# Kernel optimization log

Measured on AMD Instinct MI355X. Metric: run time of the kernel, lower is better.

## Reference

```python
import jax, jax.numpy as jnp
import numpy as np

K = 16        # max_points
S = 3         # num_scales
D_MODEL = 256
KDIM = 16
TAU = 1e-4
B_BATCH = 512


def _boundaries(k):
    edges = [(i, j) for i in range(k) for j in range(i + 1, k)]
    tris = [(i, j, kk) for i in range(k) for j in range(i + 1, k) for kk in range(j + 1, k)]
    E, T = len(edges), len(tris)
    B1 = np.zeros((k, E), np.float32)
    for e, (i, j) in enumerate(edges):
        B1[i, e] = -1.0
        B1[j, e] = 1.0
    e2i = {e: idx for idx, e in enumerate(edges)}
    B2 = np.zeros((E, T), np.float32)
    for t, (i, j, kk) in enumerate(tris):
        B2[e2i[(j, kk)], t] = 1.0
        B2[e2i[(i, kk)], t] = -1.0
        B2[e2i[(i, j)], t] = 1.0
    e_i = np.array([e[0] for e in edges], np.int32)
    e_j = np.array([e[1] for e in edges], np.int32)
    t_ij = np.array([e2i[(a, b)] for (a, b, c) in tris], np.int32)
    t_jk = np.array([e2i[(b, c)] for (a, b, c) in tris], np.int32)
    t_ik = np.array([e2i[(a, c)] for (a, b, c) in tris], np.int32)
    return B1, B2, e_i, e_j, t_ij, t_jk, t_ik


def setup_inputs() -> dict:
    key = jax.random.key(0)
    ks = jax.random.split(key, 8)
    d = D_MODEL
    B1, B2, e_i, e_j, t_ij, t_jk, t_ik = _boundaries(K)

    def lin(kk, fin, fout):
        return jax.random.normal(kk, (fin, fout), jnp.float32) / np.sqrt(fin).astype(np.float32)

    return dict(
        x=jax.random.normal(ks[0], (B_BATCH, K, d), jnp.float32),
        mask=jnp.ones((B_BATCH, K), jnp.float32),
        B1=jnp.asarray(B1), B2=jnp.asarray(B2), abs_B1=jnp.asarray(np.abs(B1)),
        e_i=jnp.asarray(e_i), e_j=jnp.asarray(e_j),
        t_ij=jnp.asarray(t_ij), t_jk=jnp.asarray(t_jk), t_ik=jnp.asarray(t_ik),
        log_scales=jnp.linspace(-1.5, 1.5, S).astype(jnp.float32),
        Wg=lin(ks[1], d, KDIM), bg=jnp.zeros((KDIM,), jnp.float32),
        Wv0=lin(ks[2], d, d * S), bv0=jnp.zeros((d * S,), jnp.float32),
        We=lin(ks[3], d, d * S), be=jnp.zeros((d * S,), jnp.float32),
        Wout=lin(ks[4], 2 * S * d, d), bout=jnp.zeros((d,), jnp.float32),
        g1=jnp.ones((d,), jnp.float32), b1=jnp.zeros((d,), jnp.float32),
        g2=jnp.ones((d,), jnp.float32), b2=jnp.zeros((d,), jnp.float32),
        Wf1=lin(ks[5], d, 4 * d), bf1=jnp.zeros((4 * d,), jnp.float32),
        Wf2=lin(ks[6], 4 * d, d), bf2=jnp.zeros((d,), jnp.float32),
    )


def _layernorm(x, g, b):
    mu = jnp.mean(x, -1, keepdims=True)
    var = jnp.mean(jnp.square(x - mu), -1, keepdims=True)
    return (x - mu) * jax.lax.rsqrt(var + 1e-5) * g + b


def _forward(x, mask, B1, B2, abs_B1, e_i, e_j, t_ij, t_jk, t_ik,
             log_scales, Wg, bg, Wv0, bv0, We, be, Wout, bout,
             g1, b1, g2, b2, Wf1, bf1, Wf2, bf2):
    B, Kp, d = x.shape
    E = B1.shape[1]
    residual = x
    x_norm = _layernorm(x, g1, b1)
    P = x_norm @ Wg + bg                                   # (B,K,k_dim)
    mask2 = mask[:, :, None] * mask[:, None, :]            # (B,K,K)
    # cdist (safe sqrt: zero diag, no NaN grads)
    pn = jnp.sum(P * P, -1)
    d2 = jnp.maximum(pn[:, :, None] + pn[:, None, :] - 2.0 * jnp.einsum('bik,bjk->bij', P, P), 0.0)
    Dm = jnp.where(d2 > 0, jnp.sqrt(jnp.where(d2 > 0, d2, 1.0)), 0.0) * mask2
    sigma_sq = jnp.square(jnp.exp(log_scales))             # (S,)
    A = jnp.exp(-(Dm * Dm)[:, None] / (2.0 * sigma_sq[None, :, None, None] + 1e-8)) * mask2[:, None]  # (B,S,K,K)
    W1 = A[:, :, e_i, e_j]                                 # (B,S,E) edge gather
    W2 = W1[:, :, t_ij] * W1[:, :, t_jk] * W1[:, :, t_ik]  # (B,S,T) triangle weights
    V0 = (x_norm @ Wv0 + bv0).reshape(B, Kp, S, d).transpose(0, 2, 1, 3)         # (B,S,K,d)
    E_raw = jnp.einsum('ke,bkd->bed', abs_B1, x_norm)                            # (B,E,d)
    E_in = (E_raw @ We + be).reshape(B, E, S, d).transpose(0, 2, 1, 3)           # (B,S,E,d)
    # L0 = B1 diag(W1) B1^T + tau I
    L0 = jnp.einsum('ke,bse,me->bskm', B1, W1, B1) + TAU * jnp.eye(Kp, dtype=x.dtype)
    M0 = jnp.einsum('bskm,bsmd->bskd', L0, V0)
    # L1 = B1^T diag(mask) B1 + B2 diag(W2) B2^T + tau I
    term_down = jnp.einsum('ke,bk,kf->bef', B1, mask, B1)                        # (B,E,E)
    term_up = jnp.einsum('et,bst,ft->bsef', B2, W2, B2)                          # (B,S,E,E)
    L1 = term_down[:, None] + term_up + TAU * jnp.eye(E, dtype=x.dtype)
    M1 = jnp.einsum('bsef,bsfd->bsed', L1, E_in)
    M1n = jnp.einsum('ke,bsed->bskd', abs_B1, M1)                                # edges -> nodes
    node_cat = M0.transpose(0, 2, 1, 3).reshape(B, Kp, S * d)
    edge_cat = M1n.transpose(0, 2, 1, 3).reshape(B, Kp, S * d)
    attn = jnp.concatenate([node_cat, edge_cat], -1) @ Wout + bout
    x2 = residual + attn                                   # dropout is identity in eval
    h = jax.nn.gelu(_layernorm(x2, g2, b2) @ Wf1 + bf1, approximate=False) @ Wf2 + bf2
    return x2 + h


def reference(x, mask, B1, B2, abs_B1, e_i, e_j, t_ij, t_jk, t_ik,
              log_scales, Wg, bg, Wv0, bv0, We, be, Wout, bout,
              g1, b1, g2, b2, Wf1, bf1, Wf2, bf2):
    return _forward(x, mask, B1, B2, abs_B1, e_i, e_j, t_ij, t_jk, t_ik,
                    log_scales, Wg, bg, Wv0, bv0, We, be, Wout, bout,
                    g1, b1, g2, b2, Wf1, bf1, Wf2, bf2)
```

## Files before the change

kernel.cpp:

```cpp
#include <hip/hip_runtime.h>
#include <math.h>

#define KN 16
#define DM 256
#define NS 3
#define NE 120
#define NT_TRI 560
#define NBATCH 512
#define TAUF 1e-4f
#define KAUG 1664
#define ZPITCH 1672

typedef unsigned short ushort_t;
typedef __attribute__((ext_vector_type(8))) short short8v;
typedef __attribute__((ext_vector_type(4))) short short4v;
typedef __attribute__((ext_vector_type(4))) float f32x4;

#define OFF_WSTACK 0u
#define OFF_WF1T   851968u
#define OFF_WF2T   1376256u
#define OFF_TOPO   1900544u
#define OFF_Z      1908736u
#define OFF_H      1908736u

__device__ __forceinline__ ushort_t f2bf(float f) {
    union { float f; unsigned int u; } v; v.f = f;
    unsigned int r = v.u + 0x7FFFu + ((v.u >> 16) & 1u);
    return (ushort_t)(r >> 16);
}
__device__ __forceinline__ void gload_lds16(const void* g, void* l) {
    auto gp = (const __attribute__((address_space(1))) unsigned int*)(unsigned long long)(g);
    auto lp = (__attribute__((address_space(3))) unsigned int*)(unsigned long long)(l);
    __builtin_amdgcn_global_load_lds(gp, lp, 16, 0, 0);
}

__global__ __launch_bounds__(256) void prep_kernel(
    const float* __restrict__ Wv0, const float* __restrict__ bv0,
    const float* __restrict__ We,  const float* __restrict__ be,
    const float* __restrict__ Wout,
    const float* __restrict__ Wf1, const float* __restrict__ Wf2,
    const int* __restrict__ e_i, const int* __restrict__ e_j,
    const int* __restrict__ t_ij, const int* __restrict__ t_jk, const int* __restrict__ t_ik,
    ushort_t* __restrict__ wstack, ushort_t* __restrict__ wf1t,
    ushort_t* __restrict__ wf2t,
    float* __restrict__ topoF, int* __restrict__ midOff, int* __restrict__ triSrt)
{
    __shared__ float lhs[16][DM];
    __shared__ float tile[64][65];
    __shared__ int   eidxL[256];
    __shared__ int   eiL[NE], ejL[NE];
    __shared__ int   midL[NT_TRI], pkL[NT_TRI];
    __shared__ int   cnts[16], offs[17];
    const int bid = blockIdx.x;
    const int j = threadIdx.x;

    if (bid == 230) {
        eidxL[j] = -1;
        if (j < NE) { eiL[j] = e_i[j]; ejL[j] = e_j[j]; }
        __syncthreads();
        if (j < NE) {
            eidxL[eiL[j]*16 + ejL[j]] = j;
            eidxL[ejL[j]*16 + eiL[j]] = j;
        }
        __syncthreads();
        const int n = j >> 4, m = j & 15;
        float q, p2, adj;
        if (n != m) {
            const int e = eidxL[j];
            if (e >= 0) { q = (m == ejL[e]) ? 1.f : -1.f; p2 = 1.f; adj = 1.f; }
            else        { q = 0.f; p2 = 0.f; adj = 0.f; }
        } else {
            q = 0.f; p2 = 0.f; adj = 0.f;
            for (int kk = 0; kk < KN; ++kk) {
                if (kk == n) continue;
                const int e = eidxL[n*16 + kk];
                if (e >= 0) { q += (n == ejL[e]) ? 1.f : -1.f; p2 += 1.f; }
            }
        }
        topoF[j] = q; topoF[256 + j] = p2; topoF[512 + j] = adj;

        for (int tt = j; tt < NT_TRI; tt += 256) {
            const int eij = t_ij[tt], ejk = t_jk[tt], eik = t_ik[tt];
            const int a0 = eiL[eij], a1 = ejL[eij];
            const int b0 = eiL[ejk], b1v = ejL[ejk];
            const int c0 = eiL[eik], c1 = ejL[eik];
            const int mid = (b0 == a0 || b0 == a1) ? b0 : b1v;
            midL[tt] = mid;
            pkL[tt]  = (a0*16 + a1) | ((b0*16 + b1v) << 8) | ((c0*16 + c1) << 16);
        }
        __syncthreads();
        if (j < 16) {
            int c = 0;
            for (int tt = 0; tt < NT_TRI; ++tt) c += (midL[tt] == j);
            cnts[j] = c;
        }
        __syncthreads();
        if (j == 0) {
            int s = 0;
            for (int q2 = 0; q2 < 16; ++q2) { offs[q2] = s; s += cnts[q2]; }
            offs[16] = s;
        }
        __syncthreads();
        if (j < 17) midOff[j] = offs[j];
        for (int tt = j; tt < NT_TRI; tt += 256) {
            const int mid = midL[tt];
            int r = 0;
            for (int q2 = 0; q2 < NT_TRI; ++q2)
                r += (q2 < tt && midL[q2] == mid);
            triSrt[offs[mid] + r] = pkL[tt];
        }
        return;
    }

    if (bid < 102) {
        const int m = bid / 17, by = bid % 17;
        const int path = m / 3, s = m % 3;
        const float* __restrict__ Wo = Wout + (size_t)m*DM*DM;
        if (by == 16) {
            const float* bv = (path == 0) ? bv0 : be;
            const float f = (path == 0) ? 1.0f : 0.5f;
            float acc = 0.f;
            for (int k = 0; k < DM; ++k)
                acc += bv[s*DM + k] * f * Wo[k*DM + j];
            wstack[(size_t)j*KAUG + 1536 + m] = f2bf(acc);
            if (m == 0)
                for (int c = 1542; c < KAUG; ++c)
                    wstack[(size_t)j*KAUG + c] = 0;
            return;
        }
        const float* src = (path == 0) ? Wv0 : We;
        const int i0 = by * 16;
        for (int r = 0; r < 16; ++r)
            lhs[r][j] = src[(size_t)(i0 + r)*(NS*DM) + s*DM + j];
        __syncthreads();
        float acc[16];
#pragma unroll
        for (int r = 0; r < 16; ++r) acc[r] = 0.f;
        for (int k = 0; k < DM; ++k) {
            const float w = Wo[k*DM + j];
#pragma unroll
            for (int r = 0; r < 16; ++r) acc[r] += lhs[r][k] * w;
        }
#pragma unroll
        for (int r = 0; r < 16; ++r)
            wstack[(size_t)j*KAUG + m*DM + i0 + r] = f2bf(acc[r]);
        return;
    }

    const float* in; ushort_t* outp; int R, C, rt, ct;
    if (bid < 166) {
        const int q = bid - 102;
        in = Wf1; outp = wf1t; R = 256; C = 1024;
        rt = (q >> 4) * 64; ct = (q & 15) * 64;
    } else {
        const int q = bid - 166;
        in = Wf2; outp = wf2t; R = 1024; C = 256;
        rt = (q >> 2) * 64; ct = (q & 3) * 64;
    }
#pragma unroll
    for (int q2 = 0; q2 < 16; ++q2) {
        const int idx = q2*256 + j;
        const int r = idx >> 6, c = idx & 63;
        tile[r][c] = in[(size_t)(rt + r)*C + ct + c];
    }
    __syncthreads();
#pragma unroll
    for (int q2 = 0; q2 < 16; ++q2) {
        const int idx = q2*256 + j;
        const int cc = idx >> 6, rr = idx & 63;
        outp[(size_t)(ct + cc)*R + rt + rr] = f2bf(tile[rr][cc]);
    }
}

__global__ __launch_bounds__(256) void topoz_kernel(
    const float* __restrict__ x, const float* __restrict__ mask,
    const float* __restrict__ log_scales,
    const float* __restrict__ Wg, const float* __restrict__ bg,
    const float* __restrict__ g1, const float* __restrict__ b1,
    const float* __restrict__ topoF, const int* __restrict__ midOff,
    const int* __restrict__ triSrt,
    ushort_t* __restrict__ Z)
{
    const int b = blockIdx.x;
    const int t = threadIdx.x;
    const int n = t >> 4, m = t & 15;

    __shared__ ushort_t xnbT[DM][16];
    __shared__ ushort_t Tbf[6][KN][16];
    __shared__ ushort_t Zstage[KN][ZPITCH];
    __shared__ float    Plds[KN][KN];
    __shared__ float    sA[NS][KN*KN];
    __shared__ float    mskL[KN];
    __shared__ int      triL[NT_TRI];
    float (*part)[NS][KN] = (float(*)[NS][KN])&Plds[0][0];

    if (t < KN) mskL[t] = mask[b*KN + t];
    for (int idx = t; idx < NT_TRI; idx += 256) triL[idx] = triSrt[idx];
    {
        const short8v z8 = {0,0,0,0,0,0,0,0};
        for (int i2 = t; i2 < 16*17; i2 += 256) {
            const int row = i2 / 17, ch = i2 % 17;
            *(short8v*)&Zstage[row][1536 + ch*8] = z8;
        }
    }

    float xv[16];
    {
        const int cg = m * 16;
        const float* xr = x + (size_t)(b*KN + n)*DM + cg;
        const f32x4 v0 = *(const f32x4*)(xr);
        const f32x4 v1 = *(const f32x4*)(xr + 4);
        const f32x4 v2 = *(const f32x4*)(xr + 8);
        const f32x4 v3 = *(const f32x4*)(xr + 12);
#pragma unroll
        for (int q = 0; q < 4; ++q) { xv[q] = v0[q]; xv[4+q] = v1[q]; xv[8+q] = v2[q]; xv[12+q] = v3[q]; }
        float ssum = 0.f;
#pragma unroll
        for (int q = 0; q < 16; ++q) ssum += xv[q];
#pragma unroll
        for (int o = 1; o < 16; o <<= 1) ssum += __shfl_xor(ssum, o);
        const float mu = ssum * (1.f/DM);
        float vsum = 0.f;
#pragma unroll
        for (int q = 0; q < 16; ++q) { const float d = xv[q]-mu; vsum += d*d; }
#pragma unroll
        for (int o = 1; o < 16; o <<= 1) vsum += __shfl_xor(vsum, o);
        const float rstd = rsqrtf(vsum*(1.f/DM) + 1e-5f);
        const f32x4 ga = *(const f32x4*)(g1 + cg),   gb = *(const f32x4*)(g1 + cg + 4);
        const f32x4 gc = *(const f32x4*)(g1 + cg + 8), gd = *(const f32x4*)(g1 + cg + 12);
        const f32x4 ba = *(const f32x4*)(b1 + cg),   bb = *(const f32x4*)(b1 + cg + 4);
        const f32x4 bc = *(const f32x4*)(b1 + cg + 8), bd = *(const f32x4*)(b1 + cg + 12);
        float gg[16], bbv[16];
#pragma unroll
        for (int q = 0; q < 4; ++q) {
            gg[q] = ga[q]; gg[4+q] = gb[q]; gg[8+q] = gc[q]; gg[12+q] = gd[q];
            bbv[q] = ba[q]; bbv[4+q] = bb[q]; bbv[8+q] = bc[q]; bbv[12+q] = bd[q];
        }
#pragma unroll
        for (int q = 0; q < 16; ++q) {
            xv[q] = (xv[q]-mu)*rstd*gg[q] + bbv[q];
            xnbT[cg + q][n] = f2bf(xv[q]);
        }
    }

    {
        float partc[16];
#pragma unroll
        for (int c = 0; c < 16; ++c) partc[c] = 0.f;
        const int cg = m * 16;
#pragma unroll
        for (int q = 0; q < 16; ++q) {
            const float xq = xv[q];
            const float* wr = Wg + (size_t)(cg + q)*KN;
            const f32x4 w0 = *(const f32x4*)(wr);
            const f32x4 w1 = *(const f32x4*)(wr + 4);
            const f32x4 w2 = *(const f32x4*)(wr + 8);
            const f32x4 w3 = *(const f32x4*)(wr + 12);
            partc[0]  += xq*w0[0]; partc[1]  += xq*w0[1]; partc[2]  += xq*w0[2]; partc[3]  += xq*w0[3];
            partc[4]  += xq*w1[0]; partc[5]  += xq*w1[1]; partc[6]  += xq*w1[2]; partc[7]  += xq*w1[3];
            partc[8]  += xq*w2[0]; partc[9]  += xq*w2[1]; partc[10] += xq*w2[2]; partc[11] += xq*w2[3];
            partc[12] += xq*w3[0]; partc[13] += xq*w3[1]; partc[14] += xq*w3[2]; partc[15] += xq*w3[3];
        }
        const int b0 = t & 1, b1b = (t>>1)&1, b2 = (t>>2)&1, b3 = (t>>3)&1;
        float p8[8];
#pragma unroll
        for (int c2 = 0; c2 < 8; ++c2) {
            const float keep = b0 ? partc[2*c2+1] : partc[2*c2];
            const float send = b0 ? partc[2*c2]   : partc[2*c2+1];
            p8[c2] = keep + __shfl_xor(send, 1);
        }
        float p4[4];
#pragma unroll
        for (int c2 = 0; c2 < 4; ++c2) {
            const float keep = b1b ? p8[2*c2+1] : p8[2*c2];
            const float send = b1b ? p8[2*c2]   : p8[2*c2+1];
            p4[c2] = keep + __shfl_xor(send, 2);
        }
        float p2v[2];
#pragma unroll
        for (int c2 = 0; c2 < 2; ++c2) {
            const float keep = b2 ? p4[2*c2+1] : p4[2*c2];
            const float send = b2 ? p4[2*c2]   : p4[2*c2+1];
            p2v[c2] = keep + __shfl_xor(send, 4);
        }
        const float keep = b3 ? p2v[1] : p2v[0];
        const float send = b3 ? p2v[0] : p2v[1];
        Plds[n][m] = keep + __shfl_xor(send, 8) + bg[m];
    }
    __syncthreads();

    float T0[NS], hq;
    {
        float d2 = 0.f;
#pragma unroll
        for (int k = 0; k < KN; ++k) {
            const float dd = Plds[n][k] - Plds[m][k];
            d2 += dd*dd;
        }
        const float m2v = mskL[n]*mskL[m];
        const float dm = (d2 > 0.f) ? sqrtf(d2)*m2v : 0.f;
        const float dmsq = dm*dm;
        const float adjv = topoF[512 + t];
#pragma unroll
        for (int s = 0; s < NS; ++s) {
            const float sig2 = __expf(2.f*log_scales[s]);
            const float a = __expf(-dmsq/(2.f*sig2 + 1e-8f)) * m2v;
            sA[s][t] = a;
            const float am = a * adjv;
            float rsum = am;
#pragma unroll
            for (int o = 1; o < 16; o <<= 1) rsum += __shfl_xor(rsum, o);
            const float tv = (m == n) ? (TAUF + rsum) : (-am);
            T0[s] = tv;
            Tbf[s][n][m] = f2bf(tv);
        }
        hq = 0.f;
#pragma unroll
        for (int k = 0; k < KN; ++k)
            hq += mskL[k]*topoF[n*16 + k]*topoF[m*16 + k];
    }
    __syncthreads();

    {
        const int c4 = t >> 6, rem = t & 63;
        const int midb = rem & 15, sb = rem >> 4;
        if (sb < NS) {
            const float* sAf = &sA[sb][0];
            float acc = 0.f;
            const int lo = midOff[midb], hi = midOff[midb + 1];
            for (int ii = lo + c4; ii < hi; ii += 4) {
                const int pk = triL[ii];
                acc += sAf[pk & 255] * sAf[(pk >> 8) & 255] * sAf[(pk >> 16) & 255];
            }
            part[c4][sb][midb] = 4.f * acc;
        }
    }
    __syncthreads();

    {
        float T1[NS];
        const float p2v = topoF[256 + t];
#pragma unroll
        for (int s = 0; s < NS; ++s) {
            float hup = 0.f;
            if (m == n)
                hup = part[0][s][n] + part[1][s][n] + part[2][s][n] + part[3][s][n];
            const float tv = hq + TAUF*p2v + hup;
            T1[s] = tv;
            Tbf[NS + s][n][m] = f2bf(tv);
        }
        float sv[6] = {T0[0], T0[1], T0[2], T1[0], T1[1], T1[2]};
#pragma unroll
        for (int q = 0; q < 6; ++q) {
            float v = sv[q];
#pragma unroll
            for (int o = 1; o < 16; o <<= 1) v += __shfl_xor(v, o);
            sv[q] = v;
        }
        const float wv = (m==0)?sv[0]:(m==1)?sv[1]:(m==2)?sv[2]:(m==3)?sv[3]:(m==4)?sv[4]:sv[5];
        if (m < 6) Zstage[n][1536 + m] = f2bf(wv);
    }
    __syncthreads();

    {
        const int w = t >> 6, l = t & 63;
        const int lr = l & 15, lk = l >> 4;
        const short8v z8 = {0,0,0,0,0,0,0,0};
        short8v bfrT[6];
#pragma unroll
        for (int m6 = 0; m6 < 6; ++m6)
            bfrT[m6] = (lk < 2) ? *(const short8v*)&Tbf[m6][lr][lk*8] : z8;
#pragma unroll
        for (int q4 = 0; q4 < 4; ++q4) {
            const int jb = w*64 + q4*16;
            const short8v axn = (lk < 2) ? *(const short8v*)&xnbT[jb + lr][lk*8] : z8;
#pragma unroll
            for (int m6 = 0; m6 < 6; ++m6) {
                f32x4 acc = {0.f,0.f,0.f,0.f};
                acc = __builtin_amdgcn_mfma_f32_16x16x32_bf16(axn, bfrT[m6], acc, 0, 0, 0);
                short4v zv;
#pragma unroll
                for (int rg = 0; rg < 4; ++rg) zv[rg] = (short)f2bf(acc[rg]);
                *(short4v*)&Zstage[lr][m6*256 + jb + lk*4] = zv;
            }
        }
    }
    __syncthreads();

    {
        ushort_t* Zb = Z + (size_t)b*KN*KAUG;
#pragma unroll
        for (int i = 0; i < 13; ++i) {
            const int cid = t + 256*i;
            const int row = cid / 208;
            const int off = (cid % 208) * 8;
            *(short8v*)(Zb + (size_t)row*KAUG + off) = *(const short8v*)&Zstage[row][off];
        }
    }
}

template<int BM, int BN, int BK, int KD, int EPI>
__global__ __launch_bounds__(256) void gemm_lds(
    const ushort_t* __restrict__ A, const ushort_t* __restrict__ Bt,
    const float* __restrict__ bias, const float* __restrict__ resid,
    float* __restrict__ outF, ushort_t* __restrict__ outH, int ldo)
{
    constexpr int ROWB = BK*2;
    constexpr int KS = BK/32;
    constexpr int MF = BM/32, NF = BN/32;
    constexpr int APASS = BM*ROWB/4096;
    constexpr int BPASS = BN*ROWB/4096;
    __shared__ ushort_t lA[BM*BK];
    __shared__ ushort_t lB[BN*BK];
    const int t = threadIdx.x;
    const int w = t >> 6, l = t & 63;
    const int wm = w & 1, wn = w >> 1;
    const int lr = l & 15, lk = l >> 4;
    const int brow = blockIdx.x * BM;
    const int bcol = blockIdx.y * BN;

    f32x4 acc[MF][NF];
#pragma unroll
    for (int mf = 0; mf < MF; ++mf)
#pragma unroll
        for (int nt = 0; nt < NF; ++nt)
            acc[mf][nt] = (f32x4){0.f,0.f,0.f,0.f};

    const int byteoff = t * 16;

    for (int kc = 0; kc < KD/BK; ++kc) {
        if (kc) __syncthreads();
#pragma unroll
        for (int c = 0; c < APASS; ++c) {
            const int bo = c*4096 + byteoff;
            const int row = bo / ROWB;
            const int gs = ((bo % ROWB) >> 4) ^ (row & 7);
            gload_lds16(A + (size_t)(brow + row)*KD + kc*BK + gs*8, lA + (bo >> 1));
        }
#pragma unroll
        for (int c = 0; c < BPASS; ++c) {
            const int bo = c*4096 + byteoff;
            const int row = bo / ROWB;
            const int gs = ((bo % ROWB) >> 4) ^ (row & 7);
            gload_lds16(Bt + (size_t)(bcol + row)*KD + kc*BK + gs*8, lB + (bo >> 1));
        }
        __syncthreads();
#pragma unroll
        for (int ks = 0; ks < KS; ++ks) {
            short8v af[MF], bfr[NF];
#pragma unroll
            for (int mf = 0; mf < MF; ++mf) {
                const int ra = wm*(BM/2) + mf*16 + lr;
                const int gs = (ks*4 + lk) ^ (ra & 7);
                af[mf] = *(const short8v*)(lA + ra*BK + gs*8);
            }
#pragma unroll
            for (int nt = 0; nt < NF; ++nt) {
                const int rb = wn*(BN/2) + nt*16 + lr;
                const int gs = (ks*4 + lk) ^ (rb & 7);
                bfr[nt] = *(const short8v*)(lB + rb*BK + gs*8);
            }
#pragma unroll
            for (int mf = 0; mf < MF; ++mf)
#pragma unroll
                for (int nt = 0; nt < NF; ++nt)
                    acc[mf][nt] = __builtin_amdgcn_mfma_f32_16x16x32_bf16(
                        af[mf], bfr[nt], acc[mf][nt], 0, 0, 0);
        }
    }

#pragma unroll
    for (int mf = 0; mf < MF; ++mf) {
#pragma unroll
        for (int nt = 0; nt < NF; ++nt) {
            const int col = bcol + wn*(BN/2) + nt*16 + lr;
#pragma unroll
            for (int rg = 0; rg < 4; ++rg) {
                const int row = brow + wm*(BM/2) + mf*16 + lk*4 + rg;
                const size_t o = (size_t)row * ldo + col;
                const float v = acc[mf][nt][rg];
                if (EPI == 2) {
                    outF[o] = outF[o] + v + bias[col];
                } else {
                    outF[o] = resid[o] + v + bias[col];
                }
            }
        }
    }
}

__global__ __launch_bounds__(256) void gemm_ffn1(
    const float* __restrict__ x2, const float* __restrict__ gv,
    const float* __restrict__ bv,
    const ushort_t* __restrict__ Bt, const float* __restrict__ bias,
    ushort_t* __restrict__ outH)
{
    constexpr int BM = 64, BN = 128, KD = 256, BK = 64, ROWB = BK*2;
    __shared__ ushort_t lnA[BM*KD];
    __shared__ ushort_t lB[BN*BK];
    const int t = threadIdx.x;
    const int w = t >> 6, l = t & 63;
    const int wm = w & 1, wn = w >> 1;
    const int lr = l & 15, lk = l >> 4;
    const int brow = blockIdx.x * BM;
    const int bcol = blockIdx.y * BN;

    {
        const int row = t >> 2, c0 = (t & 3) * 64;
        const float* xr = x2 + (size_t)(brow + row)*DM + c0;
        f32x4 va[16];
        float s = 0.f;
#pragma unroll
        for (int q = 0; q < 16; ++q) {
            va[q] = *(const f32x4*)(xr + q*4);
            s += va[q][0] + va[q][1] + va[q][2] + va[q][3];
        }
        s += __shfl_xor(s, 1); s += __shfl_xor(s, 2);
        const float mu = s * (1.f/DM);
        float vs = 0.f;
#pragma unroll
        for (int q = 0; q < 16; ++q) {
#pragma unroll
            for (int i = 0; i < 4; ++i) { const float d = va[q][i]-mu; vs += d*d; }
        }
        vs += __shfl_xor(vs, 1); vs += __shfl_xor(vs, 2);
        const float rstd = rsqrtf(vs*(1.f/DM) + 1e-5f);
#pragma unroll
        for (int q = 0; q < 16; q += 2) {
            short8v o;
#pragma unroll
            for (int i = 0; i < 4; ++i) {
                const int c = c0 + q*4 + i;
                o[i] = (short)f2bf((va[q][i]-mu)*rstd*gv[c] + bv[c]);
            }
#pragma unroll
            for (int i = 0; i < 4; ++i) {
                const int c = c0 + (q+1)*4 + i;
                o[4+i] = (short)f2bf((va[q+1][i]-mu)*rstd*gv[c] + bv[c]);
            }
            const int g = (c0 >> 3) + (q >> 1);
            const int gs = g ^ (row & 7);
            *(short8v*)(lnA + row*KD + gs*8) = o;
        }
    }

    f32x4 acc[2][4];
#pragma unroll
    for (int mf = 0; mf < 2; ++mf)
#pragma unroll
        for (int nt = 0; nt < 4; ++nt)
            acc[mf][nt] = (f32x4){0.f,0.f,0.f,0.f};

    const int byteoff = t * 16;
    for (int kc = 0; kc < KD/BK; ++kc) {
        __syncthreads();
#pragma unroll
        for (int c = 0; c < 4; ++c) {
            const int bo = c*4096 + byteoff;
            const int row = bo / ROWB;
            const int gs = ((bo % ROWB) >> 4) ^ (row & 7);
            gload_lds16(Bt + (size_t)(bcol + row)*KD + kc*BK + gs*8, lB + (bo >> 1));
        }
        __syncthreads();
#pragma unroll
        for (int ks = 0; ks < 2; ++ks) {
            short8v af[2], bfr[4];
#pragma unroll
            for (int mf = 0; mf < 2; ++mf) {
                const int ra = wm*32 + mf*16 + lr;
                const int g = kc*8 + ks*4 + lk;
                const int gs = g ^ (ra & 7);
                af[mf] = *(const short8v*)(lnA + ra*KD + gs*8);
            }
#pragma unroll
            for (int nt = 0; nt < 4; ++nt) {
                const int rb = wn*64 + nt*16 + lr;
                const int gs = (ks*4 + lk) ^ (rb & 7);
                bfr[nt] = *(const short8v*)(lB + rb*BK + gs*8);
            }
#pragma unroll
            for (int mf = 0; mf < 2; ++mf)
#pragma unroll
                for (int nt = 0; nt < 4; ++nt)
                    acc[mf][nt] = __builtin_amdgcn_mfma_f32_16x16x32_bf16(
                        af[mf], bfr[nt], acc[mf][nt], 0, 0, 0);
        }
    }

#pragma unroll
    for (int mf = 0; mf < 2; ++mf) {
#pragma unroll
        for (int nt = 0; nt < 4; ++nt) {
            const int col = bcol + wn*64 + nt*16 + lr;
#pragma unroll
            for (int rg = 0; rg < 4; ++rg) {
                const int row = brow + wm*32 + mf*16 + lk*4 + rg;
                const float u = acc[mf][nt][rg] + bias[col];
                const float a = 0.79788456080286536f*(u + 0.044715f*u*u*u);
                outH[(size_t)row*1024 + col] = f2bf(u / (1.f + __expf(-2.f*a)));
            }
        }
    }
}

extern "C" void kernel_launch(void* const* d_in, const int* in_sizes, int n_in,
                              void* d_out, int out_size, void* d_ws, size_t ws_size,
                              hipStream_t stream) {
    const float* x          = (const float*)d_in[0];
    const float* mask       = (const float*)d_in[1];
    const int*   e_i        = (const int*)  d_in[5];
    const int*   e_j        = (const int*)  d_in[6];
    const int*   t_ij       = (const int*)  d_in[7];
    const int*   t_jk       = (const int*)  d_in[8];
    const int*   t_ik       = (const int*)  d_in[9];
    const float* log_scales = (const float*)d_in[10];
    const float* Wg         = (const float*)d_in[11];
    const float* bg         = (const float*)d_in[12];
    const float* Wv0        = (const float*)d_in[13];
    const float* bv0        = (const float*)d_in[14];
    const float* We         = (const float*)d_in[15];
    const float* be         = (const float*)d_in[16];
    const float* Wout       = (const float*)d_in[17];
    const float* bout       = (const float*)d_in[18];
    const float* g1         = (const float*)d_in[19];
    const float* b1         = (const float*)d_in[20];
    const float* g2         = (const float*)d_in[21];
    const float* b2         = (const float*)d_in[22];
    const float* Wf1        = (const float*)d_in[23];
    const float* bf1        = (const float*)d_in[24];
    const float* Wf2        = (const float*)d_in[25];
    const float* bf2        = (const float*)d_in[26];

    char* wsb = (char*)d_ws;
    ushort_t* wstack = (ushort_t*)(wsb + OFF_WSTACK);
    ushort_t* wf1t   = (ushort_t*)(wsb + OFF_WF1T);
    ushort_t* wf2t   = (ushort_t*)(wsb + OFF_WF2T);
    float*    topoF  = (float*)   (wsb + OFF_TOPO);
    int*      midOff = (int*)     (wsb + OFF_TOPO + 3072);
    int*      triSrt = (int*)     (wsb + OFF_TOPO + 3200);
    ushort_t* Z      = (ushort_t*)(wsb + OFF_Z);
    ushort_t* H      = (ushort_t*)(wsb + OFF_H);
    float*    out    = (float*)d_out;

    hipLaunchKernelGGL(prep_kernel, dim3(231), dim3(256), 0, stream,
                       Wv0, bv0, We, be, Wout, Wf1, Wf2,
                       e_i, e_j, t_ij, t_jk, t_ik,
                       wstack, wf1t, wf2t, topoF, midOff, triSrt);
    hipLaunchKernelGGL(topoz_kernel, dim3(NBATCH), dim3(256), 0, stream,
                       x, mask, log_scales, Wg, bg, g1, b1,
                       topoF, midOff, triSrt, Z);
    hipLaunchKernelGGL((gemm_lds<64,64,128,KAUG,3>), dim3(128,4), dim3(256), 0, stream,
                       Z, wstack, bout, x, out, (ushort_t*)nullptr, 256);
    hipLaunchKernelGGL(gemm_ffn1, dim3(128,8), dim3(256), 0, stream,
                       out, g2, b2, wf1t, bf1, H);
    hipLaunchKernelGGL((gemm_lds<64,64,128,1024,2>), dim3(128,4), dim3(256), 0, stream,
                       H, wf2t, bf2, (const float*)nullptr,
                       out, (ushort_t*)nullptr, 256);
}
```

Measured before the change: 131.1 us.

## Fuse attention output projection into topology kernel, dropping Z intermediate and GEMM

The topology kernel previously wrote a large augmented Z matrix (T·xn per scale plus row sums) to global memory, and a separate GEMM multiplied it by the stacked Wout-folded weights. Now each batch block computes xn·Wcat directly with MFMA, reading the folded weights from global, stages the result in LDS, and multiplies by the concatenated T operators. Row-sum bias terms are applied in fp32 before the block writes x2 with the residual. This removes the Z round trip and one kernel launch. In exchange, every one of the 512 blocks re-reads the full 768 KB weight matrix, relying on L2 reuse, and does more serialized per-block work.

```diff
diff --git a/kernel.cpp b/kernel.cpp
--- a/kernel.cpp
+++ b/kernel.cpp
@@ -8,20 +8,20 @@
 #define NT_TRI 560
 #define NBATCH 512
 #define TAUF 1e-4f
-#define KAUG 1664
-#define ZPITCH 1672
+#define XPITCH 264
+#define TPITCH 104
 
 typedef unsigned short ushort_t;
 typedef __attribute__((ext_vector_type(8))) short short8v;
 typedef __attribute__((ext_vector_type(4))) short short4v;
 typedef __attribute__((ext_vector_type(4))) float f32x4;
 
-#define OFF_WSTACK 0u
-#define OFF_WF1T   851968u
-#define OFF_WF2T   1376256u
-#define OFF_TOPO   1900544u
-#define OFF_Z      1908736u
-#define OFF_H      1908736u
+#define OFF_WCAT   0u
+#define OFF_BIASF  786432u
+#define OFF_WF1T   792576u
+#define OFF_WF2T   1316864u
+#define OFF_TOPO   1841152u
+#define OFF_H      1900544u
 
 __device__ __forceinline__ ushort_t f2bf(float f) {
     union { float f; unsigned int u; } v; v.f = f;
@@ -41,8 +41,8 @@
     const float* __restrict__ Wf1, const float* __restrict__ Wf2,
     const int* __restrict__ e_i, const int* __restrict__ e_j,
     const int* __restrict__ t_ij, const int* __restrict__ t_jk, const int* __restrict__ t_ik,
-    ushort_t* __restrict__ wstack, ushort_t* __restrict__ wf1t,
-    ushort_t* __restrict__ wf2t,
+    ushort_t* __restrict__ wcat, float* __restrict__ biasf,
+    ushort_t* __restrict__ wf1t, ushort_t* __restrict__ wf2t,
     float* __restrict__ topoF, int* __restrict__ midOff, int* __restrict__ triSrt)
 {
     __shared__ float lhs[16][DM];
@@ -122,10 +122,7 @@
             float acc = 0.f;
             for (int k = 0; k < DM; ++k)
                 acc += bv[s*DM + k] * f * Wo[k*DM + j];
-            wstack[(size_t)j*KAUG + 1536 + m] = f2bf(acc);
-            if (m == 0)
-                for (int c = 1542; c < KAUG; ++c)
-                    wstack[(size_t)j*KAUG + c] = 0;
+            biasf[m*DM + j] = acc;
             return;
         }
         const float* src = (path == 0) ? Wv0 : We;
@@ -143,7 +140,7 @@
         }
 #pragma unroll
         for (int r = 0; r < 16; ++r)
-            wstack[(size_t)j*KAUG + m*DM + i0 + r] = f2bf(acc[r]);
+            wcat[(size_t)(m*DM + j)*DM + i0 + r] = f2bf(acc[r]);
         return;
     }
 
@@ -172,37 +169,33 @@
     }
 }
 
-__global__ __launch_bounds__(256) void topoz_kernel(
+__global__ __launch_bounds__(256) void topoy_kernel(
     const float* __restrict__ x, const float* __restrict__ mask,
     const float* __restrict__ log_scales,
     const float* __restrict__ Wg, const float* __restrict__ bg,
     const float* __restrict__ g1, const float* __restrict__ b1,
     const float* __restrict__ topoF, const int* __restrict__ midOff,
     const int* __restrict__ triSrt,
-    ushort_t* __restrict__ Z)
+    const ushort_t* __restrict__ wcat, const float* __restrict__ biasf,
+    const float* __restrict__ bout,
+    float* __restrict__ x2out)
 {
     const int b = blockIdx.x;
     const int t = threadIdx.x;
     const int n = t >> 4, m = t & 15;
 
-    __shared__ ushort_t xnbT[DM][16];
-    __shared__ ushort_t Tbf[6][KN][16];
-    __shared__ ushort_t Zstage[KN][ZPITCH];
+    __shared__ ushort_t xnb[KN][XPITCH];
+    __shared__ ushort_t Tcat[KN][TPITCH];
+    __shared__ ushort_t ychunk[64][TPITCH];
     __shared__ float    Plds[KN][KN];
     __shared__ float    sA[NS][KN*KN];
+    __shared__ float    rsL[6][KN];
     __shared__ float    mskL[KN];
     __shared__ int      triL[NT_TRI];
     float (*part)[NS][KN] = (float(*)[NS][KN])&Plds[0][0];
 
     if (t < KN) mskL[t] = mask[b*KN + t];
     for (int idx = t; idx < NT_TRI; idx += 256) triL[idx] = triSrt[idx];
-    {
-        const short8v z8 = {0,0,0,0,0,0,0,0};
-        for (int i2 = t; i2 < 16*17; i2 += 256) {
-            const int row = i2 / 17, ch = i2 % 17;
-            *(short8v*)&Zstage[row][1536 + ch*8] = z8;
-        }
-    }
 
     float xv[16];
     {
@@ -236,11 +229,14 @@
             gg[q] = ga[q]; gg[4+q] = gb[q]; gg[8+q] = gc[q]; gg[12+q] = gd[q];
             bbv[q] = ba[q]; bbv[4+q] = bb[q]; bbv[8+q] = bc[q]; bbv[12+q] = bd[q];
         }
+        short8v o0, o1;
 #pragma unroll
         for (int q = 0; q < 16; ++q) {
             xv[q] = (xv[q]-mu)*rstd*gg[q] + bbv[q];
-            xnbT[cg + q][n] = f2bf(xv[q]);
-        }
+            if (q < 8) o0[q] = (short)f2bf(xv[q]); else o1[q-8] = (short)f2bf(xv[q]);
+        }
+        *(short8v*)&xnb[n][cg]     = o0;
+        *(short8v*)&xnb[n][cg + 8] = o1;
     }
 
     {
@@ -289,7 +285,7 @@
     }
     __syncthreads();
 
-    float T0[NS], hq;
+    float hq;
     {
         float d2 = 0.f;
 #pragma unroll
@@ -301,6 +297,7 @@
         const float dm = (d2 > 0.f) ? sqrtf(d2)*m2v : 0.f;
         const float dmsq = dm*dm;
         const float adjv = topoF[512 + t];
+        float T0[NS];
 #pragma unroll
         for (int s = 0; s < NS; ++s) {
             const float sig2 = __expf(2.f*log_scales[s]);
@@ -312,12 +309,19 @@
             for (int o = 1; o < 16; o <<= 1) rsum += __shfl_xor(rsum, o);
             const float tv = (m == n) ? (TAUF + rsum) : (-am);
             T0[s] = tv;
-            Tbf[s][n][m] = f2bf(tv);
+            Tcat[n][s*16 + m] = f2bf(tv);
         }
         hq = 0.f;
 #pragma unroll
         for (int k = 0; k < KN; ++k)
             hq += mskL[k]*topoF[n*16 + k]*topoF[m*16 + k];
+#pragma unroll
+        for (int s = 0; s < NS; ++s) {
+            float v = T0[s];
+#pragma unroll
+            for (int o = 1; o < 16; o <<= 1) v += __shfl_xor(v, o);
+            if (m == s) rsL[s][n] = v;
+        }
     }
     __syncthreads();
 
@@ -338,7 +342,6 @@
     __syncthreads();
 
     {
-        float T1[NS];
         const float p2v = topoF[256 + t];
 #pragma unroll
         for (int s = 0; s < NS; ++s) {
@@ -346,56 +349,64 @@
             if (m == n)
                 hup = part[0][s][n] + part[1][s][n] + part[2][s][n] + part[3][s][n];
             const float tv = hq + TAUF*p2v + hup;
-            T1[s] = tv;
-            Tbf[NS + s][n][m] = f2bf(tv);
-        }
-        float sv[6] = {T0[0], T0[1], T0[2], T1[0], T1[1], T1[2]};
-#pragma unroll
-        for (int q = 0; q < 6; ++q) {
-            float v = sv[q];
+            Tcat[n][(NS + s)*16 + m] = f2bf(tv);
+            float v = tv;
 #pragma unroll
             for (int o = 1; o < 16; o <<= 1) v += __shfl_xor(v, o);
-            sv[q] = v;
-        }
-        const float wv = (m==0)?sv[0]:(m==1)?sv[1]:(m==2)?sv[2]:(m==3)?sv[3]:(m==4)?sv[4]:sv[5];
-        if (m < 6) Zstage[n][1536 + m] = f2bf(wv);
+            if (m == NS + s) rsL[NS + s][n] = v;
+        }
     }
     __syncthreads();
 
-    {
-        const int w = t >> 6, l = t & 63;
-        const int lr = l & 15, lk = l >> 4;
-        const short8v z8 = {0,0,0,0,0,0,0,0};
-        short8v bfrT[6];
-#pragma unroll
-        for (int m6 = 0; m6 < 6; ++m6)
-            bfrT[m6] = (lk < 2) ? *(const short8v*)&Tbf[m6][lr][lk*8] : z8;
-#pragma unroll
-        for (int q4 = 0; q4 < 4; ++q4) {
-            const int jb = w*64 + q4*16;
-            const short8v axn = (lk < 2) ? *(const short8v*)&xnbT[jb + lr][lk*8] : z8;
+    const int w = t >> 6, l = t & 63;
+    const int lr = l & 15, lk = l >> 4;
+    short8v axn[8];
+#pragma unroll
+    for (int kc = 0; kc < 8; ++kc)
+        axn[kc] = *(const short8v*)&xnb[lr][kc*32 + lk*8];
+
+    for (int jc = 0; jc < 4; ++jc) {
+#pragma unroll
+        for (int m6 = 0; m6 < 6; ++m6) {
+            const ushort_t* wp = wcat + (size_t)(m6*DM + jc*64 + w*16 + lr)*DM + lk*8;
+            f32x4 acc = {0.f,0.f,0.f,0.f};
+#pragma unroll
+            for (int kc = 0; kc < 8; ++kc) {
+                const short8v bw = *(const short8v*)(wp + kc*32);
+                acc = __builtin_amdgcn_mfma_f32_16x16x32_bf16(axn[kc], bw, acc, 0, 0, 0);
+            }
+            short4v yv;
+#pragma unroll
+            for (int rg = 0; rg < 4; ++rg) yv[rg] = (short)f2bf(acc[rg]);
+            *(short4v*)&ychunk[w*16 + lr][m6*16 + lk*4] = yv;
+        }
+        __syncthreads();
+
+        f32x4 sacc = {0.f,0.f,0.f,0.f};
+#pragma unroll
+        for (int kc3 = 0; kc3 < 3; ++kc3) {
+            const short8v ay = *(const short8v*)&ychunk[w*16 + lr][kc3*32 + lk*8];
+            const short8v bt = *(const short8v*)&Tcat[lr][kc3*32 + lk*8];
+            sacc = __builtin_amdgcn_mfma_f32_16x16x32_bf16(ay, bt, sacc, 0, 0, 0);
+        }
+        {
+            const int nrow = lr;
+            const int j0 = jc*64 + w*16 + lk*4;
+            const f32x4 xv4 = *(const f32x4*)(x + (size_t)(b*KN + nrow)*DM + j0);
+            const f32x4 bo4 = *(const f32x4*)(bout + j0);
+            f32x4 ab = {0.f,0.f,0.f,0.f};
 #pragma unroll
             for (int m6 = 0; m6 < 6; ++m6) {
-                f32x4 acc = {0.f,0.f,0.f,0.f};
-                acc = __builtin_amdgcn_mfma_f32_16x16x32_bf16(axn, bfrT[m6], acc, 0, 0, 0);
-                short4v zv;
-#pragma unroll
-                for (int rg = 0; rg < 4; ++rg) zv[rg] = (short)f2bf(acc[rg]);
-                *(short4v*)&Zstage[lr][m6*256 + jb + lk*4] = zv;
-            }
-        }
-    }
-    __syncthreads();
-
-    {
-        ushort_t* Zb = Z + (size_t)b*KN*KAUG;
-#pragma unroll
-        for (int i = 0; i < 13; ++i) {
-            const int cid = t + 256*i;
-            const int row = cid / 208;
-            const int off = (cid % 208) * 8;
-            *(short8v*)(Zb + (size_t)row*KAUG + off) = *(const short8v*)&Zstage[row][off];
-        }
+                const f32x4 bf4 = *(const f32x4*)(biasf + m6*DM + j0);
+                const float r = rsL[m6][nrow];
+                ab[0] += r*bf4[0]; ab[1] += r*bf4[1]; ab[2] += r*bf4[2]; ab[3] += r*bf4[3];
+            }
+            f32x4 o;
+#pragma unroll
+            for (int i = 0; i < 4; ++i) o[i] = xv4[i] + sacc[i] + ab[i] + bo4[i];
+            *(f32x4*)(x2out + (size_t)(b*KN + nrow)*DM + j0) = o;
+        }
+        __syncthreads();
     }
 }
 
@@ -478,12 +489,7 @@
             for (int rg = 0; rg < 4; ++rg) {
                 const int row = brow + wm*(BM/2) + mf*16 + lk*4 + rg;
                 const size_t o = (size_t)row * ldo + col;
-                const float v = acc[mf][nt][rg];
-                if (EPI == 2) {
-                    outF[o] = outF[o] + v + bias[col];
-                } else {
-                    outF[o] = resid[o] + v + bias[col];
-                }
+                outF[o] = outF[o] + acc[mf][nt][rg] + bias[col];
             }
         }
     }
@@ -632,25 +638,23 @@
     const float* bf2        = (const float*)d_in[26];
 
     char* wsb = (char*)d_ws;
-    ushort_t* wstack = (ushort_t*)(wsb + OFF_WSTACK);
+    ushort_t* wcat   = (ushort_t*)(wsb + OFF_WCAT);
+    float*    biasf  = (float*)   (wsb + OFF_BIASF);
     ushort_t* wf1t   = (ushort_t*)(wsb + OFF_WF1T);
     ushort_t* wf2t   = (ushort_t*)(wsb + OFF_WF2T);
     float*    topoF  = (float*)   (wsb + OFF_TOPO);
     int*      midOff = (int*)     (wsb + OFF_TOPO + 3072);
     int*      triSrt = (int*)     (wsb + OFF_TOPO + 3200);
-    ushort_t* Z      = (ushort_t*)(wsb + OFF_Z);
     ushort_t* H      = (ushort_t*)(wsb + OFF_H);
     float*    out    = (float*)d_out;
 
     hipLaunchKernelGGL(prep_kernel, dim3(231), dim3(256), 0, stream,
                        Wv0, bv0, We, be, Wout, Wf1, Wf2,
                        e_i, e_j, t_ij, t_jk, t_ik,
-                       wstack, wf1t, wf2t, topoF, midOff, triSrt);
-    hipLaunchKernelGGL(topoz_kernel, dim3(NBATCH), dim3(256), 0, stream,
+                       wcat, biasf, wf1t, wf2t, topoF, midOff, triSrt);
+    hipLaunchKernelGGL(topoy_kernel, dim3(NBATCH), dim3(256), 0, stream,
                        x, mask, log_scales, Wg, bg, g1, b1,
-                       topoF, midOff, triSrt, Z);
-    hipLaunchKernelGGL((gemm_lds<64,64,128,KAUG,3>), dim3(128,4), dim3(256), 0, stream,
-                       Z, wstack, bout, x, out, (ushort_t*)nullptr, 256);
+                       topoF, midOff, triSrt, wcat, biasf, bout, out);
     hipLaunchKernelGGL(gemm_ffn1, dim3(128,8), dim3(256), 0, stream,
                        out, g2, b2, wf1t, bf1, H);
     hipLaunchKernelGGL((gemm_lds<64,64,128,1024,2>), dim3(128,4), dim3(256), 0, stream,
```

Result: slower. 164.5 us (+25.5%).
